# Kernel tuning notes

Measured on AMD Instinct MI355X. Metric: run time of the kernel, lower is better.

## Reference

```python
import jax, jax.numpy as jnp
import numpy as np

SIGMA = 0.1  # init kwarg sigma
B_CONST = 1.0  # init kwarg b
EPS = 1e-5


def setup_inputs() -> dict:
    key = jax.random.key(0)
    k1, k2 = jax.random.split(key)
    shape = (4, 256, 48, 48)  # N, C, H, W
    return {
        "featureT": jax.random.normal(k1, shape, dtype=jnp.float32),
        "featureI": jax.random.normal(k2, shape, dtype=jnp.float32),
    }


def reference(featureT, featureI):
    # center both features by the target's per-channel mean (over N, H, W)
    meanT = featureT.mean(axis=(0, 2, 3), keepdims=True)
    fI = featureI - meanT
    fT = featureT - meanT
    # l2-normalize channelwise (dim=1)
    fI = fI / jnp.linalg.norm(fI, axis=1, keepdims=True)
    fT = fT / jnp.linalg.norm(fT, axis=1, keepdims=True)
    N, C, H, W = fT.shape
    P = H * W
    # per-sample all-pairs patch cosine similarity: dist[n,p,h,w] = sum_c fT[n,c,p] * fI[n,c,h,w]
    # (equivalent to the per-sample F.conv2d with 1x1 filters from patch_decomposition)
    dist = jnp.einsum('ncp,nchw->nphw', fT.reshape(N, C, P), fI)  # [N, P, H, W]
    raw_dist = (1.0 - dist) / 2.0
    # relative distances along the patch axis (axis=1)
    div = jnp.min(raw_dist, axis=1, keepdims=True)
    relative_dist = raw_dist / (div + EPS)
    # contextual similarity: exp-weighted normalization along axis=1
    Wmat = jnp.exp((B_CONST - relative_dist) / SIGMA)
    CX = Wmat / jnp.sum(Wmat, axis=1, keepdims=True)
    # max over spatial dims (3 then 2), mean over patches
    CX = CX.max(axis=(2, 3))  # [N, P]
    CX = CX.mean(axis=1)      # [N]
    CX_B = -jnp.log(CX)       # [N]
    loss = jnp.mean(CX_B)
    return (loss, CX_B)
```

## Files before the change

kernel.cpp:

```cpp
#include <hip/hip_runtime.h>
#include <hip/hip_fp16.h>

#define NN 4
#define CC 256
#define PP 2304
#define EPSV 1e-5f

typedef __attribute__((ext_vector_type(8))) short bf16x8;
typedef __attribute__((ext_vector_type(4))) float f32x4;

struct alignas(8) h4 { __half2 a, b; };

__device__ inline unsigned fenc(float f) {
  unsigned b = __float_as_uint(f);
  return (b & 0x80000000u) ? ~b : (b | 0x80000000u);
}
__device__ inline float fdec(unsigned e) {
  unsigned b = (e & 0x80000000u) ? (e ^ 0x80000000u) : ~e;
  return __uint_as_float(b);
}

__device__ inline unsigned short f2bf(float x) {
  unsigned u = __float_as_uint(x);
  unsigned r = (u + 0x7FFFu + ((u >> 16) & 1u)) >> 16;
  return (unsigned short)r;
}

__device__ inline void gload_lds16(const unsigned short* g, unsigned short* l) {
  __builtin_amdgcn_global_load_lds(
      (const __attribute__((address_space(1))) void*)g,
      (__attribute__((address_space(3))) void*)l, 16, 0, 0);
}

__global__ __launch_bounds__(256) void k_mean(const float* __restrict__ fT,
                                              float* __restrict__ partial,
                                              unsigned* __restrict__ divu,
                                              float* __restrict__ cxsum) {
  int c = blockIdx.x, n = blockIdx.y, t = threadIdx.x;
  const float4* base = (const float4*)(fT + ((size_t)n * CC + c) * PP);
  float s = 0.f;
  for (int k = t; k < 576; k += 256) {
    float4 v = base[k];
    s += (v.x + v.y) + (v.z + v.w);
  }
  for (int o = 32; o > 0; o >>= 1) s += __shfl_down(s, o);
  __shared__ float red[4];
  if ((t & 63) == 0) red[t >> 6] = s;
  __syncthreads();
  if (t == 0) partial[c * NN + n] = red[0] + red[1] + red[2] + red[3];
  if (n == 0 && t < 36) divu[c * 36 + t] = 0xFFFFFFFFu;
  if (n == 0 && c == 0 && t < 4) cxsum[t] = 0.f;
}

__global__ __launch_bounds__(256) void k_norm(const float* __restrict__ fT,
                                              const float* __restrict__ fI,
                                              const float* __restrict__ partial,
                                              unsigned short* __restrict__ A,
                                              unsigned short* __restrict__ B) {
  int n = blockIdx.y;
  int p0 = blockIdx.x * 16;
  int t = threadIdx.x;
  int pq = (t & 3) * 4;
  int cg = t >> 2;
  __shared__ float cT[16][257];
  __shared__ float cI[16][257];
  __shared__ float redf[2][16][65];
  __shared__ float inv[2][16];
  float aT[4] = {0.f, 0.f, 0.f, 0.f}, aI[4] = {0.f, 0.f, 0.f, 0.f};
#pragma unroll
  for (int ph = 0; ph < 4; ph++) {
    int c = ph * 64 + cg;
    float m = (partial[c * NN + 0] + partial[c * NN + 1] +
               partial[c * NN + 2] + partial[c * NN + 3]) * (1.0f / (float)(NN * PP));
    size_t g = ((size_t)n * CC + c) * PP + p0 + pq;
    float4 vT = *(const float4*)(fT + g);
    float4 vI = *(const float4*)(fI + g);
    float xT[4] = {vT.x - m, vT.y - m, vT.z - m, vT.w - m};
    float xI[4] = {vI.x - m, vI.y - m, vI.z - m, vI.w - m};
#pragma unroll
    for (int k = 0; k < 4; k++) {
      cT[pq + k][c] = xT[k]; cI[pq + k][c] = xI[k];
      aT[k] += xT[k] * xT[k]; aI[k] += xI[k] * xI[k];
    }
  }
#pragma unroll
  for (int k = 0; k < 4; k++) {
    redf[0][pq + k][cg] = aT[k];
    redf[1][pq + k][cg] = aI[k];
  }
  __syncthreads();
  if (t < 32) {
    int which = t >> 4, p = t & 15;
    float s = 0.f;
    for (int g = 0; g < 64; g++) s += redf[which][p][g];
    inv[which][p] = 1.0f / sqrtf(s);
  }
  __syncthreads();
#pragma unroll
  for (int it = 0; it < 2; it++) {
    int task = it * 256 + t;
    int ps = task >> 5;
    int ch = task & 31;
    float iA = inv[0][ps], iB = inv[1][ps];
    unsigned short va[8], vb[8];
#pragma unroll
    for (int e = 0; e < 8; e++) {
      va[e] = f2bf(cT[ps][ch * 8 + e] * iA);
      vb[e] = f2bf(cI[ps][ch * 8 + e] * iB);
    }
    size_t o = ((size_t)(n * PP + p0 + ps)) * CC + ch * 8;
    *(int4*)(A + o) = *(const int4*)va;
    *(int4*)(B + o) = *(const int4*)vb;
  }
}

__global__ __launch_bounds__(256) void k_gemm(const unsigned short* __restrict__ A,
                                              const unsigned short* __restrict__ B,
                                              __half* __restrict__ rawt,
                                              unsigned* __restrict__ divu) {
  int n  = blockIdx.z;
  int i0 = blockIdx.y * 128;
  int j0 = blockIdx.x * 128;
  int t  = threadIdx.x;
  int lane = t & 63;
  int w = t >> 6;
  int wi = w >> 1, wj = w & 1;
  int lr = lane & 15, lq = lane >> 4;

  __shared__ __align__(16) char smem[33792];
  unsigned short* As = (unsigned short*)smem;
  unsigned short* Bs = (unsigned short*)(smem + 16384);
  __half* r16t = (__half*)smem;
  __shared__ unsigned cmin[128];
  if (t < 128) cmin[t] = 0xFFFFFFFFu;

  f32x4 acc[4][4];
#pragma unroll
  for (int a = 0; a < 4; a++)
#pragma unroll
    for (int b = 0; b < 4; b++) acc[a][b] = (f32x4){0.f, 0.f, 0.f, 0.f};

  const size_t baseA = ((size_t)(n * PP + i0)) * CC;
  const size_t baseB = ((size_t)(n * PP + j0)) * CC;
  int lrow8 = lane >> 3;
  int lseg  = (lane & 7) ^ (lrow8 & 7);

  for (int k0 = 0; k0 < CC; k0 += 64) {
    if (k0) __syncthreads();
#pragma unroll
    for (int it = 0; it < 4; it++) {
      int sb = (w * 4 + it) * 64;
      int row = (w * 4 + it) * 8 + lrow8;
      gload_lds16(A + baseA + (size_t)row * CC + k0 + lseg * 8, As + sb * 8);
      gload_lds16(B + baseB + (size_t)row * CC + k0 + lseg * 8, Bs + sb * 8);
    }
    __syncthreads();
#pragma unroll
    for (int ks = 0; ks < 2; ks++) {
      bf16x8 af[4], bf[4];
#pragma unroll
      for (int ti = 0; ti < 4; ti++) {
        int row = wi * 64 + ti * 16 + lr;
        int slot = row * 8 + ((ks * 4 + lq) ^ (lr & 7));
        af[ti] = *(const bf16x8*)&As[slot * 8];
      }
#pragma unroll
      for (int tj = 0; tj < 4; tj++) {
        int row = wj * 64 + tj * 16 + lr;
        int slot = row * 8 + ((ks * 4 + lq) ^ (lr & 7));
        bf[tj] = *(const bf16x8*)&Bs[slot * 8];
      }
#pragma unroll
      for (int ti = 0; ti < 4; ti++)
#pragma unroll
        for (int tj = 0; tj < 4; tj++)
          acc[ti][tj] = __builtin_amdgcn_mfma_f32_16x16x32_bf16(af[ti], bf[tj], acc[ti][tj], 0, 0, 0);
    }
  }

  __syncthreads();
#pragma unroll
  for (int tj = 0; tj < 4; tj++) {
    float mx = -1e30f;
    int cj = wj * 64 + tj * 16 + lr;
#pragma unroll
    for (int ti = 0; ti < 4; ti++) {
      alignas(8) unsigned short pk[4];
#pragma unroll
      for (int r = 0; r < 4; r++) {
        float g = acc[ti][tj][r];
        mx = fmaxf(mx, g);
        pk[r] = __half_as_ushort(__float2half((1.0f - g) * 0.5f));
      }
      int ci = wi * 64 + ti * 16 + lq * 4;
      *(short4*)&r16t[cj * 132 + ci] = *(const short4*)pk;
    }
    atomicMin(&cmin[cj], fenc((1.0f - mx) * 0.5f));
  }
  __syncthreads();
#pragma unroll
  for (int m = 0; m < 8; m++) {
    int chunk = m * 256 + t;
    int row = chunk >> 4, cs = chunk & 15;
    int2 lo = *(const int2*)&r16t[row * 132 + cs * 8];
    int2 hi = *(const int2*)&r16t[row * 132 + cs * 8 + 4];
    int4 v = {lo.x, lo.y, hi.x, hi.y};
    *(int4*)(rawt + ((size_t)(n * PP + j0 + row)) * PP + i0 + cs * 8) = v;
  }
  if (t < 128) atomicMin(&divu[n * PP + j0 + t], cmin[t]);
}

__global__ __launch_bounds__(256) void k_colsum(const __half* __restrict__ rawt,
                                                const unsigned* __restrict__ divu,
                                                float* __restrict__ scale,
                                                float* __restrict__ lnS) {
  int t = threadIdx.x, lane = t & 63, w = t >> 6;
  int r = blockIdx.x * 4 + w;
  float d = fdec(divu[r]);
  float sc = -10.0f / (d + EPSV);
  const __half* rp = rawt + (size_t)r * PP;
  float s = 0.f;
#pragma unroll
  for (int c = 0; c < 9; c++) {
    h4 hv = *(const h4*)(rp + c * 256 + lane * 4);
    float2 f01 = __half22float2(hv.a);
    float2 f23 = __half22float2(hv.b);
    s += __expf(f01.x * sc) + __expf(f01.y * sc) + __expf(f23.x * sc) + __expf(f23.y * sc);
  }
  for (int o = 32; o > 0; o >>= 1) s += __shfl_down(s, o);
  if (lane == 0) {
    scale[r] = sc;
    lnS[r] = logf(s);
  }
}

__global__ __launch_bounds__(512) void k_rowmax(const __half* __restrict__ rawt,
                                                const float* __restrict__ scale,
                                                const float* __restrict__ lnS,
                                                float* __restrict__ cxsum) {
  int n = blockIdx.y;
  int i0 = blockIdx.x * 32;
  int t = threadIdx.x, lane = t & 63, w = t >> 6;
  int q = t & 7, g = t >> 3;
  int i = i0 + q * 4;
  const float* scp = scale + n * PP;
  const float* lnp = lnS + n * PP;
  float m0 = -1e30f, m1 = -1e30f, m2 = -1e30f, m3 = -1e30f;
#pragma unroll 4
  for (int it = 0; it < 36; it++) {
    int j = it * 64 + g;
    float scj = scp[j], lsj = lnp[j];
    h4 hv = *(const h4*)(rawt + ((size_t)(n * PP + j)) * PP + i);
    float2 f01 = __half22float2(hv.a);
    float2 f23 = __half22float2(hv.b);
    m0 = fmaxf(m0, fmaf(f01.x, scj, -lsj));
    m1 = fmaxf(m1, fmaf(f01.y, scj, -lsj));
    m2 = fmaxf(m2, fmaf(f23.x, scj, -lsj));
    m3 = fmaxf(m3, fmaf(f23.y, scj, -lsj));
  }
#pragma unroll
  for (int o = 8; o <= 32; o <<= 1) {
    m0 = fmaxf(m0, __shfl_xor(m0, o));
    m1 = fmaxf(m1, __shfl_xor(m1, o));
    m2 = fmaxf(m2, __shfl_xor(m2, o));
    m3 = fmaxf(m3, __shfl_xor(m3, o));
  }
  __shared__ float4 red[8][8];
  if (lane < 8) red[w][lane] = (float4){m0, m1, m2, m3};
  __syncthreads();
  if (t < 8) {
    float4 a = red[0][t];
#pragma unroll
    for (int ww = 1; ww < 8; ww++) {
      float4 b = red[ww][t];
      a.x = fmaxf(a.x, b.x); a.y = fmaxf(a.y, b.y);
      a.z = fmaxf(a.z, b.z); a.w = fmaxf(a.w, b.w);
    }
    float v = (__expf(a.x) + __expf(a.y) + __expf(a.z) + __expf(a.w)) * (1.0f / (float)PP);
    v += __shfl_down(v, 4);
    v += __shfl_down(v, 2);
    v += __shfl_down(v, 1);
    if (t == 0) atomicAdd(&cxsum[n], v);
  }
}

__global__ void k_final(const float* __restrict__ cxsum, float* __restrict__ out) {
  int t = threadIdx.x;
  float cxb = 0.f;
  if (t < 4) {
    cxb = -logf(cxsum[t]);
    out[1 + t] = cxb;
  }
  for (int o = 2; o > 0; o >>= 1) cxb += __shfl_down(cxb, o);
  if (t == 0) out[0] = cxb * 0.25f;
}

extern "C" void kernel_launch(void* const* d_in, const int* in_sizes, int n_in,
                              void* d_out, int out_size, void* d_ws, size_t ws_size,
                              hipStream_t stream) {
  const float* fT = (const float*)d_in[0];
  const float* fI = (const float*)d_in[1];
  float* out = (float*)d_out;

  char* w = (char*)d_ws;
  float* partial = (float*)w;
  unsigned* divu = (unsigned*)(w + 4096);
  float* scale   = (float*)(w + 4096 + 36864);
  float* lnS     = (float*)(w + 4096 + 2 * 36864);
  float* cxsum   = (float*)(w + 4096 + 3 * 36864);
  size_t off = 4096 + 3 * 36864 + 1024;
  unsigned short* A = (unsigned short*)(w + off);
  unsigned short* B = (unsigned short*)(w + off + 4718592);
  __half* rawt = (__half*)(w + off + 2 * 4718592);

  k_mean<<<dim3(CC, NN), 256, 0, stream>>>(fT, partial, divu, cxsum);
  k_norm<<<dim3(PP / 16, NN), 256, 0, stream>>>(fT, fI, partial, A, B);
  k_gemm<<<dim3(PP / 128, PP / 128, NN), 256, 0, stream>>>(A, B, rawt, divu);
  k_colsum<<<dim3(PP * NN / 4), 256, 0, stream>>>(rawt, divu, scale, lnS);
  k_rowmax<<<dim3(PP / 32, NN), 512, 0, stream>>>(rawt, scale, lnS, cxsum);
  k_final<<<1, 64, 0, stream>>>(cxsum, out);
}
```

Baseline: 126.6 us.

## Widen fp16 loads in colsum/rowmax and fold final reduction into rowmax

Column-sum and row-max kernels now read 8 halves (16 bytes) per thread instead of 4, which halves the load instruction count and loop trips. The separate single-block final kernel is removed. Instead, the last rowmax block, found through an atomic counter and a threadfence, computes the log terms and writes the outputs. This saves one kernel launch at the cost of a grid-wide atomic completion counter that has to be reset each call.

```diff
diff --git a/kernel.cpp b/kernel.cpp
--- a/kernel.cpp
+++ b/kernel.cpp
@@ -10,6 +10,7 @@
 typedef __attribute__((ext_vector_type(4))) float f32x4;
 
 struct alignas(8) h4 { __half2 a, b; };
+struct alignas(16) h8 { __half2 a, b, c, d; };
 
 __device__ inline unsigned fenc(float f) {
   unsigned b = __float_as_uint(f);
@@ -35,7 +36,8 @@
 __global__ __launch_bounds__(256) void k_mean(const float* __restrict__ fT,
                                               float* __restrict__ partial,
                                               unsigned* __restrict__ divu,
-                                              float* __restrict__ cxsum) {
+                                              float* __restrict__ cxsum,
+                                              unsigned* __restrict__ counter) {
   int c = blockIdx.x, n = blockIdx.y, t = threadIdx.x;
   const float4* base = (const float4*)(fT + ((size_t)n * CC + c) * PP);
   float s = 0.f;
@@ -50,6 +52,7 @@
   if (t == 0) partial[c * NN + n] = red[0] + red[1] + red[2] + red[3];
   if (n == 0 && t < 36) divu[c * 36 + t] = 0xFFFFFFFFu;
   if (n == 0 && c == 0 && t < 4) cxsum[t] = 0.f;
+  if (n == 0 && c == 0 && t == 4) *counter = 0u;
 }
 
 __global__ __launch_bounds__(256) void k_norm(const float* __restrict__ fT,
@@ -221,10 +224,16 @@
   const __half* rp = rawt + (size_t)r * PP;
   float s = 0.f;
 #pragma unroll
-  for (int c = 0; c < 9; c++) {
-    h4 hv = *(const h4*)(rp + c * 256 + lane * 4);
-    float2 f01 = __half22float2(hv.a);
-    float2 f23 = __half22float2(hv.b);
+  for (int c = 0; c < 4; c++) {
+    h8 hv = *(const h8*)(rp + c * 512 + lane * 8);
+    float2 f0 = __half22float2(hv.a), f1 = __half22float2(hv.b);
+    float2 f2 = __half22float2(hv.c), f3 = __half22float2(hv.d);
+    s += __expf(f0.x * sc) + __expf(f0.y * sc) + __expf(f1.x * sc) + __expf(f1.y * sc);
+    s += __expf(f2.x * sc) + __expf(f2.y * sc) + __expf(f3.x * sc) + __expf(f3.y * sc);
+  }
+  {
+    h4 hv = *(const h4*)(rp + 2048 + lane * 4);
+    float2 f01 = __half22float2(hv.a), f23 = __half22float2(hv.b);
     s += __expf(f01.x * sc) + __expf(f01.y * sc) + __expf(f23.x * sc) + __expf(f23.y * sc);
   }
   for (int o = 32; o > 0; o >>= 1) s += __shfl_down(s, o);
@@ -237,62 +246,68 @@
 __global__ __launch_bounds__(512) void k_rowmax(const __half* __restrict__ rawt,
                                                 const float* __restrict__ scale,
                                                 const float* __restrict__ lnS,
-                                                float* __restrict__ cxsum) {
+                                                float* __restrict__ cxsum,
+                                                unsigned* __restrict__ counter,
+                                                float* __restrict__ out) {
   int n = blockIdx.y;
   int i0 = blockIdx.x * 32;
   int t = threadIdx.x, lane = t & 63, w = t >> 6;
-  int q = t & 7, g = t >> 3;
-  int i = i0 + q * 4;
+  int q = lane & 3;
+  int g = w * 16 + (lane >> 2);
+  int i = i0 + q * 8;
   const float* scp = scale + n * PP;
   const float* lnp = lnS + n * PP;
-  float m0 = -1e30f, m1 = -1e30f, m2 = -1e30f, m3 = -1e30f;
-#pragma unroll 4
-  for (int it = 0; it < 36; it++) {
-    int j = it * 64 + g;
+  float m[8];
+#pragma unroll
+  for (int e = 0; e < 8; e++) m[e] = -1e30f;
+#pragma unroll 2
+  for (int it = 0; it < 18; it++) {
+    int j = it * 128 + g;
     float scj = scp[j], lsj = lnp[j];
-    h4 hv = *(const h4*)(rawt + ((size_t)(n * PP + j)) * PP + i);
-    float2 f01 = __half22float2(hv.a);
-    float2 f23 = __half22float2(hv.b);
-    m0 = fmaxf(m0, fmaf(f01.x, scj, -lsj));
-    m1 = fmaxf(m1, fmaf(f01.y, scj, -lsj));
-    m2 = fmaxf(m2, fmaf(f23.x, scj, -lsj));
-    m3 = fmaxf(m3, fmaf(f23.y, scj, -lsj));
-  }
-#pragma unroll
-  for (int o = 8; o <= 32; o <<= 1) {
-    m0 = fmaxf(m0, __shfl_xor(m0, o));
-    m1 = fmaxf(m1, __shfl_xor(m1, o));
-    m2 = fmaxf(m2, __shfl_xor(m2, o));
-    m3 = fmaxf(m3, __shfl_xor(m3, o));
-  }
-  __shared__ float4 red[8][8];
-  if (lane < 8) red[w][lane] = (float4){m0, m1, m2, m3};
-  __syncthreads();
-  if (t < 8) {
-    float4 a = red[0][t];
-#pragma unroll
-    for (int ww = 1; ww < 8; ww++) {
-      float4 b = red[ww][t];
-      a.x = fmaxf(a.x, b.x); a.y = fmaxf(a.y, b.y);
-      a.z = fmaxf(a.z, b.z); a.w = fmaxf(a.w, b.w);
-    }
-    float v = (__expf(a.x) + __expf(a.y) + __expf(a.z) + __expf(a.w)) * (1.0f / (float)PP);
-    v += __shfl_down(v, 4);
-    v += __shfl_down(v, 2);
-    v += __shfl_down(v, 1);
-    if (t == 0) atomicAdd(&cxsum[n], v);
-  }
-}
-
-__global__ void k_final(const float* __restrict__ cxsum, float* __restrict__ out) {
-  int t = threadIdx.x;
-  float cxb = 0.f;
-  if (t < 4) {
-    cxb = -logf(cxsum[t]);
-    out[1 + t] = cxb;
-  }
-  for (int o = 2; o > 0; o >>= 1) cxb += __shfl_down(cxb, o);
-  if (t == 0) out[0] = cxb * 0.25f;
+    h8 hv = *(const h8*)(rawt + ((size_t)(n * PP + j)) * PP + i);
+    float2 f0 = __half22float2(hv.a), f1 = __half22float2(hv.b);
+    float2 f2 = __half22float2(hv.c), f3 = __half22float2(hv.d);
+    m[0] = fmaxf(m[0], fmaf(f0.x, scj, -lsj));
+    m[1] = fmaxf(m[1], fmaf(f0.y, scj, -lsj));
+    m[2] = fmaxf(m[2], fmaf(f1.x, scj, -lsj));
+    m[3] = fmaxf(m[3], fmaf(f1.y, scj, -lsj));
+    m[4] = fmaxf(m[4], fmaf(f2.x, scj, -lsj));
+    m[5] = fmaxf(m[5], fmaf(f2.y, scj, -lsj));
+    m[6] = fmaxf(m[6], fmaf(f3.x, scj, -lsj));
+    m[7] = fmaxf(m[7], fmaf(f3.y, scj, -lsj));
+  }
+#pragma unroll
+  for (int o = 4; o <= 32; o <<= 1)
+#pragma unroll
+    for (int e = 0; e < 8; e++) m[e] = fmaxf(m[e], __shfl_xor(m[e], o));
+  __shared__ float red[8][4][8];
+  if (lane < 4)
+#pragma unroll
+    for (int e = 0; e < 8; e++) red[w][lane][e] = m[e];
+  __syncthreads();
+  if (t < 32) {
+    int qq = t >> 3, e = t & 7;
+    float M = red[0][qq][e];
+#pragma unroll
+    for (int ww = 1; ww < 8; ww++) M = fmaxf(M, red[ww][qq][e]);
+    float v = __expf(M) * (1.0f / (float)PP);
+    v += __shfl_down(v, 16); v += __shfl_down(v, 8);
+    v += __shfl_down(v, 4);  v += __shfl_down(v, 2); v += __shfl_down(v, 1);
+    if (t == 0) {
+      atomicAdd(&cxsum[n], v);
+      __threadfence();
+      unsigned done = atomicAdd(counter, 1u);
+      if (done == (unsigned)(gridDim.x * gridDim.y - 1)) {
+        float c0 = atomicAdd(&cxsum[0], 0.f);
+        float c1 = atomicAdd(&cxsum[1], 0.f);
+        float c2 = atomicAdd(&cxsum[2], 0.f);
+        float c3 = atomicAdd(&cxsum[3], 0.f);
+        float l0 = -logf(c0), l1 = -logf(c1), l2 = -logf(c2), l3 = -logf(c3);
+        out[0] = 0.25f * (l0 + l1 + l2 + l3);
+        out[1] = l0; out[2] = l1; out[3] = l2; out[4] = l3;
+      }
+    }
+  }
 }
 
 extern "C" void kernel_launch(void* const* d_in, const int* in_sizes, int n_in,
@@ -308,15 +323,15 @@
   float* scale   = (float*)(w + 4096 + 36864);
   float* lnS     = (float*)(w + 4096 + 2 * 36864);
   float* cxsum   = (float*)(w + 4096 + 3 * 36864);
+  unsigned* counter = (unsigned*)(w + 4096 + 3 * 36864 + 64);
   size_t off = 4096 + 3 * 36864 + 1024;
   unsigned short* A = (unsigned short*)(w + off);
   unsigned short* B = (unsigned short*)(w + off + 4718592);
   __half* rawt = (__half*)(w + off + 2 * 4718592);
 
-  k_mean<<<dim3(CC, NN), 256, 0, stream>>>(fT, partial, divu, cxsum);
+  k_mean<<<dim3(CC, NN), 256, 0, stream>>>(fT, partial, divu, cxsum, counter);
   k_norm<<<dim3(PP / 16, NN), 256, 0, stream>>>(fT, fI, partial, A, B);
   k_gemm<<<dim3(PP / 128, PP / 128, NN), 256, 0, stream>>>(A, B, rawt, divu);
   k_colsum<<<dim3(PP * NN / 4), 256, 0, stream>>>(rawt, divu, scale, lnS);
-  k_rowmax<<<dim3(PP / 32, NN), 512, 0, stream>>>(rawt, scale, lnS, cxsum);
-  k_final<<<1, 64, 0, stream>>>(cxsum, out);
-}
+  k_rowmax<<<dim3(PP / 32, NN), 512, 0, stream>>>(rawt, scale, lnS, cxsum, counter, out);
+}
```

New measurement: 131.0 us. +3.4%, slower.
